# Performance work log

Measured on AMD Instinct MI355X. Metric: run time of the kernel, lower is better.

The kernel has to match this reference:

```python
import jax, jax.numpy as jnp
import numpy as np

B, T, D, U = 32, 512, 512, 512  # batch, seq_len, input dim, lstm units


def setup_inputs() -> dict:
    key = jax.random.key(0)
    ks = jax.random.split(key, 8)
    s_in = 1.0 / np.sqrt(D)
    s_rec = 1.0 / np.sqrt(U)
    return {
        "x": jax.random.normal(ks[0], (B, T, D), dtype=jnp.float32),
        "z": jax.random.normal(ks[1], (B, U), dtype=jnp.float32) * 0.1,
        # forward-direction LSTM params (Keras gate order: i, f, c, o)
        "Wf": jax.random.normal(ks[2], (D, 4 * U), dtype=jnp.float32) * s_in,
        "Uf": jax.random.normal(ks[3], (U, 4 * U), dtype=jnp.float32) * s_rec,
        "bf": jnp.zeros((4 * U,), dtype=jnp.float32),
        # backward-direction LSTM params
        "Wb": jax.random.normal(ks[4], (D, 4 * U), dtype=jnp.float32) * s_in,
        "Ub": jax.random.normal(ks[5], (U, 4 * U), dtype=jnp.float32) * s_rec,
        "bb": jnp.zeros((4 * U,), dtype=jnp.float32),
    }


def _lstm(x, h0, c0, W, Uw, b, reverse):
    """Single-direction LSTM, return_sequences=True. Keras gate order i,f,c,o."""
    u = h0.shape[-1]
    # precompute input projections for all timesteps in one big GEMM
    xg = jnp.einsum("btd,dk->btk", x, W) + b  # [B,T,4U]

    def step(carry, xg_t):
        h, c = carry
        g = xg_t + h @ Uw  # [B,4U]
        i = jax.nn.sigmoid(g[:, :u])
        f = jax.nn.sigmoid(g[:, u:2 * u])
        cc = jnp.tanh(g[:, 2 * u:3 * u])
        o = jax.nn.sigmoid(g[:, 3 * u:])
        c = f * c + i * cc
        h = o * jnp.tanh(c)
        return (h, c), h

    # scan over time; reverse=True == Keras go_backwards + output re-reversal
    _, hs = jax.lax.scan(step, (h0, c0), jnp.swapaxes(xg, 0, 1), reverse=reverse)
    return jnp.swapaxes(hs, 0, 1)  # [B,T,U]


def reference(x, z, Wf, Uf, bf, Wb, Ub, bb):
    # conditional=True: initial_state = [z, z, z, z] -> both directions get (h0=z, c0=z)
    fwd = _lstm(x, z, z, Wf, Uf, bf, reverse=False)
    bwd = _lstm(x, z, z, Wb, Ub, bb, reverse=True)
    return fwd + bwd  # Bidirectional merge_mode='sum', return_sequences=True
```

## Files before the change

### kernel.cpp

```cpp
#include <hip/hip_runtime.h>
#include <hip/hip_bf16.h>


typedef __attribute__((ext_vector_type(8))) __bf16 bf16x8;
typedef __attribute__((ext_vector_type(4))) __bf16 bf16x4;
typedef __attribute__((ext_vector_type(4))) float fvec4;

#define AS_G(p) ((const __attribute__((address_space(1))) void*)(p))
#define AS_L(p) ((__attribute__((address_space(3))) void*)(p))

__device__ __forceinline__ float sigm(float x) {
  return __builtin_amdgcn_rcpf(1.f + __expf(-x));
}
__device__ __forceinline__ float tanh_f(float x) {
  return 1.f - 2.f * __builtin_amdgcn_rcpf(__expf(2.f * x) + 1.f);
}

__device__ __forceinline__ void st_h4(__bf16* p, float h0, float h1) {
  union { __bf16 h[2]; unsigned int u; } pk;
  pk.h[0] = (__bf16)h0;
  pk.h[1] = (__bf16)h1;
  __hip_atomic_store((unsigned int*)p, pk.u, __ATOMIC_RELAXED, __HIP_MEMORY_SCOPE_AGENT);
}


__global__ void k_convert_x(const float* __restrict__ x, __bf16* __restrict__ xb) {
  size_t i = ((size_t)blockIdx.x * 256 + threadIdx.x) * 8;
  fvec4 a = *(const fvec4*)(x + i);
  fvec4 b = *(const fvec4*)(x + i + 4);
  bf16x8 o;
#pragma unroll
  for (int j = 0; j < 4; ++j) { o[j] = (__bf16)a[j]; o[4 + j] = (__bf16)b[j]; }
  *(bf16x8*)(xb + i) = o;
}

__global__ void k_build_T(const float* __restrict__ src, const float* __restrict__ bvec,
                          __bf16* __restrict__ dst, float* __restrict__ bias_out) {
  int p = blockIdx.x;
  int g = p >> 6, r = p & 63, w = r >> 4, q = r & 15, jj = q >> 2, gate = q & 3;
  int orig = gate * 512 + g * 16 + w * 4 + jj;
  for (int k = threadIdx.x; k < 512; k += 256)
    dst[(size_t)p * 512 + k] = (__bf16)src[(size_t)k * 2048 + orig];
  if (bias_out && threadIdx.x == 0) bias_out[p] = bvec[orig];
}

__global__ void k_init_flags(int* mbox) {
  int i = blockIdx.x * 256 + threadIdx.x;
  if (i < 2048) mbox[i] = 0;
}

__global__ void k_init_h(const float* __restrict__ z, __bf16* __restrict__ hbuf) {
  int idx = blockIdx.x * 256 + threadIdx.x;
  int dir = idx >> 14, rem = idx & 16383;
  int ks = rem >> 10, row = (rem >> 5) & 31, c = rem & 31;
  hbuf[(size_t)dir * 32768 + rem] = (__bf16)z[row * 512 + ks * 32 + c];
}


__global__ __launch_bounds__(256, 2) void k_gemm_xw(
    const __bf16* __restrict__ A,
    const __bf16* __restrict__ Bt,
    const float* __restrict__ bias,
    __bf16* __restrict__ C)
{
  __shared__ __align__(16) __bf16 As[128 * 32];
  __shared__ __align__(16) __bf16 Bs[128 * 32];
  const int tid = threadIdx.x;
  const int w = tid >> 6, lane = tid & 63, quad = lane >> 4, l15 = lane & 15;
  const int m0 = blockIdx.y * 128, n0 = blockIdx.x * 128;
  const int wm = w & 1, wn = w >> 1;

  fvec4 acc[4][4];
  const fvec4 zero = {0.f, 0.f, 0.f, 0.f};
#pragma unroll
  for (int i = 0; i < 4; ++i)
#pragma unroll
    for (int j = 0; j < 4; ++j) acc[i][j] = zero;

  for (int kb = 0; kb < 16; ++kb) {
    const int k0 = kb * 32;
#pragma unroll
    for (int i = 0; i < 2; ++i) {
      const int c = (i * 4 + w) * 64 + lane;
      const int row = c >> 2, kk = (c & 3) * 8;
      __builtin_amdgcn_global_load_lds(AS_G(A + (size_t)(m0 + row) * 512 + k0 + kk),
                                       AS_L(As + (size_t)(i * 4 + w) * 512), 16, 0, 0);
      __builtin_amdgcn_global_load_lds(AS_G(Bt + (size_t)(n0 + row) * 512 + k0 + kk),
                                       AS_L(Bs + (size_t)(i * 4 + w) * 512), 16, 0, 0);
    }
    __syncthreads();
    bf16x8 af[4], bfr[4];
#pragma unroll
    for (int mt = 0; mt < 4; ++mt)
      af[mt] = *(const bf16x8*)(As + (wm * 64 + mt * 16 + l15) * 32 + quad * 8);
#pragma unroll
    for (int nt = 0; nt < 4; ++nt)
      bfr[nt] = *(const bf16x8*)(Bs + (wn * 64 + nt * 16 + l15) * 32 + quad * 8);
#pragma unroll
    for (int mt = 0; mt < 4; ++mt)
#pragma unroll
      for (int nt = 0; nt < 4; ++nt)
        acc[mt][nt] = __builtin_amdgcn_mfma_f32_16x16x32_bf16(af[mt], bfr[nt], acc[mt][nt], 0, 0, 0);
    __syncthreads();
  }

#pragma unroll
  for (int nt = 0; nt < 4; ++nt) {
    const int col = n0 + wn * 64 + nt * 16 + l15;
    const float bv = bias[col];
#pragma unroll
    for (int mt = 0; mt < 4; ++mt) {
      const int rowb = m0 + wm * 64 + mt * 16 + quad * 4;
#pragma unroll
      for (int r = 0; r < 4; ++r)
        C[(size_t)(rowb + r) * 4096 + col] = (__bf16)(acc[mt][nt][r] + bv);
    }
  }
}


__global__ __launch_bounds__(256, 1) void k_lstm_rec(
    const __bf16* __restrict__ xg,
    const float* __restrict__ z,
    const __bf16* __restrict__ UT,
    __bf16* __restrict__ hbuf,
    float* __restrict__ outf,
    __bf16* __restrict__ outb,
    int* __restrict__ mbox)
{
  const int blk = blockIdx.x, dir = blk >> 5, g = blk & 31;
  const int tid = threadIdx.x, w = tid >> 6, lane = tid & 63;
  const int quad = lane >> 4, l15 = lane & 15;
  __shared__ __align__(16) __bf16 h_lds[16384];
  __shared__ __align__(16) float gates[32][68];

  bf16x8 breg[16];
  {
    const __bf16* up = UT + ((size_t)dir * 2048 + g * 64 + w * 16 + l15) * 512 + quad * 8;
#pragma unroll
    for (int ks = 0; ks < 16; ++ks) breg[ks] = *(const bf16x8*)(up + ks * 32);
  }

  const int b = lane >> 1, jpair = lane & 1;
  const int hcol = g * 16 + w * 4 + jpair * 2;
  float c0 = z[b * 512 + hcol];
  float c1 = z[b * 512 + hcol + 1];
  const __bf16* hsrc = hbuf + (size_t)dir * 32768;
  const int stoff = (g >> 1) * 1024 + b * 32 + (g & 1) * 16 + w * 4 + jpair * 2;
  const int stage_off = w * 4096 + lane * 8;
  const int swz8 = ((lane & 3) ^ ((lane >> 3) & 3)) * 8;
  const int fr_swz = ((l15 >> 1) & 3);
  int* my_line = mbox + dir * 1024 + g * 32;
  int* my_col  = mbox + dir * 1024 + lane * 32 + g;
  const fvec4 zero = {0.f, 0.f, 0.f, 0.f};

  for (int kt = 0; kt < 512; ++kt) {
    const int t = dir ? (511 - kt) : kt;
    const int pr = kt & 1;

    const bf16x8 xv = *(const bf16x8*)(xg + (size_t)(b * 512 + t) * 4096 +
                                       dir * 2048 + g * 64 + w * 16 + jpair * 8);

    if (kt > 0) {
      if (w == 0) {
        const int* mb = my_line + (lane & 31);
        for (;;) {
          int v = __hip_atomic_load(mb, __ATOMIC_RELAXED, __HIP_MEMORY_SCOPE_AGENT);
          if (!__ballot(lane < 32 && v < kt)) break;
          __builtin_amdgcn_s_sleep(1);
        }
      }
      __syncthreads();
    }

    {
      const unsigned long long* src =
          (const unsigned long long*)(hsrc + pr * 16384 + stage_off);
      unsigned long long tmp[16];
#pragma unroll
      for (int it = 0; it < 8; ++it) {
        tmp[2 * it]     = __hip_atomic_load(src + it * 128,
                            __ATOMIC_RELAXED, __HIP_MEMORY_SCOPE_AGENT);
        tmp[2 * it + 1] = __hip_atomic_load(src + it * 128 + 1,
                            __ATOMIC_RELAXED, __HIP_MEMORY_SCOPE_AGENT);
      }
#pragma unroll
      for (int it = 0; it < 8; ++it) {
        union { unsigned long long u[2]; bf16x8 v; } cv;
        cv.u[0] = tmp[2 * it];
        cv.u[1] = tmp[2 * it + 1];
        *(bf16x8*)(h_lds + (w * 4 + (it >> 1)) * 1024 +
                   ((it & 1) * 16 + (lane >> 2)) * 32 + swz8) = cv.v;
      }
    }
    __syncthreads();

    fvec4 acc0 = zero, acc1 = zero;
#pragma unroll 8
    for (int ks = 0; ks < 16; ++ks) {
      bf16x8 a0 = *(const bf16x8*)(h_lds + ks * 1024 + l15 * 32 +
                                   ((quad ^ fr_swz) * 8));
      bf16x8 a1 = *(const bf16x8*)(h_lds + ks * 1024 + (16 + l15) * 32 +
                                   ((quad ^ fr_swz) * 8));
      acc0 = __builtin_amdgcn_mfma_f32_16x16x32_bf16(a0, breg[ks], acc0, 0, 0, 0);
      acc1 = __builtin_amdgcn_mfma_f32_16x16x32_bf16(a1, breg[ks], acc1, 0, 0, 0);
    }

#pragma unroll
    for (int r = 0; r < 4; ++r) {
      gates[quad * 4 + r][w * 16 + l15] = acc0[r];
      gates[16 + quad * 4 + r][w * 16 + l15] = acc1[r];
    }
    const fvec4 gA = *(const fvec4*)&gates[b][w * 16 + jpair * 8];
    const fvec4 gB = *(const fvec4*)&gates[b][w * 16 + jpair * 8 + 4];

    float xf[8];
#pragma unroll
    for (int j = 0; j < 8; ++j) xf[j] = (float)xv[j];

    float ii = sigm(gA[0] + xf[0]);
    float ff = sigm(gA[1] + xf[1]);
    float cc = tanh_f(gA[2] + xf[2]);
    float oo = sigm(gA[3] + xf[3]);
    c0 = ff * c0 + ii * cc;
    const float h0 = oo * tanh_f(c0);

    ii = sigm(gB[0] + xf[4]);
    ff = sigm(gB[1] + xf[5]);
    cc = tanh_f(gB[2] + xf[6]);
    oo = sigm(gB[3] + xf[7]);
    c1 = ff * c1 + ii * cc;
    const float h1 = oo * tanh_f(c1);

    st_h4(hbuf + (size_t)dir * 32768 + ((kt + 1) & 1) * 16384 + stoff, h0, h1);

    __syncthreads();
    if (w == 0 && lane < 32)
      __hip_atomic_store(my_col, kt + 1, __ATOMIC_RELAXED, __HIP_MEMORY_SCOPE_AGENT);

    const size_t oidx = (size_t)(b * 512 + t) * 512 + hcol;
    if (dir == 0) {
      outf[oidx] = h0;
      outf[oidx + 1] = h1;
    } else {
      outb[oidx] = (__bf16)h0;
      outb[oidx + 1] = (__bf16)h1;
    }
  }
}


__global__ void k_add_bwd(float* __restrict__ out, const __bf16* __restrict__ outb) {
  size_t i = ((size_t)blockIdx.x * 256 + threadIdx.x) * 4;
  if (i >= (size_t)32 * 512 * 512) return;
  fvec4 o = *(const fvec4*)(out + i);
  bf16x4 bv = *(const bf16x4*)(outb + i);
#pragma unroll
  for (int j = 0; j < 4; ++j) o[j] += (float)bv[j];
  *(fvec4*)(out + i) = o;
}


extern "C" void kernel_launch(void* const* d_in, const int* in_sizes, int n_in,
                              void* d_out, int out_size, void* d_ws, size_t ws_size,
                              hipStream_t stream) {
  const float* x  = (const float*)d_in[0];
  const float* z  = (const float*)d_in[1];
  const float* Wf = (const float*)d_in[2];
  const float* Uf = (const float*)d_in[3];
  const float* bf = (const float*)d_in[4];
  const float* Wb = (const float*)d_in[5];
  const float* Ub = (const float*)d_in[6];
  const float* bb = (const float*)d_in[7];
  float* out = (float*)d_out;
  char* ws = (char*)d_ws;

  size_t off = 0;
  __bf16* xg    = (__bf16*)(ws + off); off += (size_t)16384 * 4096 * 2;
  __bf16* UT    = (__bf16*)(ws + off); off += (size_t)2 * 2048 * 512 * 2;
  __bf16* hbuf  = (__bf16*)(ws + off); off += (size_t)2 * 2 * 16384 * 2;
  int*    mbox  = (int*)(ws + off);    off += 8192;
  float*  biasp = (float*)(ws + off);  off += 4096 * 4;
  char* uni = ws + off;
  __bf16* xb   = (__bf16*)uni;
  __bf16* WT   = (__bf16*)(uni + (size_t)16384 * 512 * 2);
  __bf16* outb = (__bf16*)uni;

  k_convert_x<<<4096, 256, 0, stream>>>(x, xb);
  k_build_T<<<2048, 256, 0, stream>>>(Wf, bf, WT, biasp);
  k_build_T<<<2048, 256, 0, stream>>>(Wb, bb, WT + (size_t)2048 * 512, biasp + 2048);
  k_build_T<<<2048, 256, 0, stream>>>(Uf, nullptr, UT, nullptr);
  k_build_T<<<2048, 256, 0, stream>>>(Ub, nullptr, UT + (size_t)2048 * 512, nullptr);
  k_init_flags<<<8, 256, 0, stream>>>(mbox);
  k_init_h<<<128, 256, 0, stream>>>(z, hbuf);
  k_gemm_xw<<<dim3(32, 128), 256, 0, stream>>>(xb, WT, biasp, xg);
  k_lstm_rec<<<64, 256, 0, stream>>>(xg, z, UT, hbuf, out, outb, mbox);
  k_add_bwd<<<8192, 256, 0, stream>>>(out, outb);
}
```

Baseline: 2.205 ms.

## Replace flag mailbox sync with step-tagged h values in recurrent LSTM kernel

Drops the separate per-block flag mailbox and the extra barrier-then-flag-store handshake. Each 64-bit store now carries the packed bf16 h pair together with the timestep counter, so consumers poll the data words directly until every tag matches the expected step. This takes a polling round trip and a __syncthreads off each of the 512 serial steps. In exchange the exchanged buffer doubles in size, every thread spins on 32 global loads per step, and the LDS layout changes to a padded, unswizzled one that may bring bank conflicts.

Result: slower. 2.770 ms (+25.6%).

```diff
diff --git a/kernel.cpp b/kernel.cpp
--- a/kernel.cpp
+++ b/kernel.cpp
@@ -5,6 +5,7 @@
 typedef __attribute__((ext_vector_type(8))) __bf16 bf16x8;
 typedef __attribute__((ext_vector_type(4))) __bf16 bf16x4;
 typedef __attribute__((ext_vector_type(4))) float fvec4;
+typedef __attribute__((ext_vector_type(2))) float fvec2;
 
 #define AS_G(p) ((const __attribute__((address_space(1))) void*)(p))
 #define AS_L(p) ((__attribute__((address_space(3))) void*)(p))
@@ -14,13 +15,6 @@
 }
 __device__ __forceinline__ float tanh_f(float x) {
   return 1.f - 2.f * __builtin_amdgcn_rcpf(__expf(2.f * x) + 1.f);
-}
-
-__device__ __forceinline__ void st_h4(__bf16* p, float h0, float h1) {
-  union { __bf16 h[2]; unsigned int u; } pk;
-  pk.h[0] = (__bf16)h0;
-  pk.h[1] = (__bf16)h1;
-  __hip_atomic_store((unsigned int*)p, pk.u, __ATOMIC_RELAXED, __HIP_MEMORY_SCOPE_AGENT);
 }
 
 
@@ -44,16 +38,19 @@
   if (bias_out && threadIdx.x == 0) bias_out[p] = bvec[orig];
 }
 
-__global__ void k_init_flags(int* mbox) {
-  int i = blockIdx.x * 256 + threadIdx.x;
-  if (i < 2048) mbox[i] = 0;
-}
-
-__global__ void k_init_h(const float* __restrict__ z, __bf16* __restrict__ hbuf) {
+__global__ void k_init_rec(const float* __restrict__ z,
+                           unsigned long long* __restrict__ rbuf) {
   int idx = blockIdx.x * 256 + threadIdx.x;
-  int dir = idx >> 14, rem = idx & 16383;
-  int ks = rem >> 10, row = (rem >> 5) & 31, c = rem & 31;
-  hbuf[(size_t)dir * 32768 + rem] = (__bf16)z[row * 512 + ks * 32 + c];
+  int par = (idx >> 13) & 1;
+  int ks = (idx >> 9) & 15, row = (idx >> 4) & 31, cp = idx & 15;
+  unsigned long long v = 0ull;
+  if (par == 0) {
+    union { __bf16 h[2]; unsigned u; } pk;
+    pk.h[0] = (__bf16)z[row * 512 + ks * 32 + cp * 2];
+    pk.h[1] = (__bf16)z[row * 512 + ks * 32 + cp * 2 + 1];
+    v = (unsigned long long)pk.u;
+  }
+  rbuf[idx] = v;
 }
 
 
@@ -123,15 +120,14 @@
     const __bf16* __restrict__ xg,
     const float* __restrict__ z,
     const __bf16* __restrict__ UT,
-    __bf16* __restrict__ hbuf,
+    unsigned long long* __restrict__ rbuf,
     float* __restrict__ outf,
-    __bf16* __restrict__ outb,
-    int* __restrict__ mbox)
+    __bf16* __restrict__ outb)
 {
   const int blk = blockIdx.x, dir = blk >> 5, g = blk & 31;
   const int tid = threadIdx.x, w = tid >> 6, lane = tid & 63;
   const int quad = lane >> 4, l15 = lane & 15;
-  __shared__ __align__(16) __bf16 h_lds[16384];
+  __shared__ __align__(16) char h_lds[16 * 2080];
   __shared__ __align__(16) float gates[32][68];
 
   bf16x8 breg[16];
@@ -145,63 +141,50 @@
   const int hcol = g * 16 + w * 4 + jpair * 2;
   float c0 = z[b * 512 + hcol];
   float c1 = z[b * 512 + hcol + 1];
-  const __bf16* hsrc = hbuf + (size_t)dir * 32768;
-  const int stoff = (g >> 1) * 1024 + b * 32 + (g & 1) * 16 + w * 4 + jpair * 2;
-  const int stage_off = w * 4096 + lane * 8;
-  const int swz8 = ((lane & 3) ^ ((lane >> 3) & 3)) * 8;
-  const int fr_swz = ((l15 >> 1) & 3);
-  int* my_line = mbox + dir * 1024 + g * 32;
-  int* my_col  = mbox + dir * 1024 + lane * 32 + g;
-  const fvec4 zero = {0.f, 0.f, 0.f, 0.f};
+
+  const int ks_s = tid >> 4, cp = tid & 15;
+  unsigned long long* rb_dir = rbuf + (size_t)dir * 16384;
+  unsigned long long* src_base = rb_dir + ks_s * 512 + cp;
+  const int pidx = (g >> 1) * 512 + b * 16 + (g & 1) * 8 + w * 2 + jpair;
 
   for (int kt = 0; kt < 512; ++kt) {
     const int t = dir ? (511 - kt) : kt;
     const int pr = kt & 1;
 
+    asm volatile("s_waitcnt lgkmcnt(0)\n\ts_barrier" ::: "memory");
+
     const bf16x8 xv = *(const bf16x8*)(xg + (size_t)(b * 512 + t) * 4096 +
                                        dir * 2048 + g * 64 + w * 16 + jpair * 8);
 
-    if (kt > 0) {
-      if (w == 0) {
-        const int* mb = my_line + (lane & 31);
-        for (;;) {
-          int v = __hip_atomic_load(mb, __ATOMIC_RELAXED, __HIP_MEMORY_SCOPE_AGENT);
-          if (!__ballot(lane < 32 && v < kt)) break;
-          __builtin_amdgcn_s_sleep(1);
-        }
+    unsigned long long rec[32];
+    {
+      unsigned long long* srcp = src_base + pr * 8192;
+      const unsigned expect = (unsigned)kt;
+      for (;;) {
+#pragma unroll
+        for (int it = 0; it < 32; ++it)
+          rec[it] = __hip_atomic_load(srcp + it * 16, __ATOMIC_RELAXED,
+                                      __HIP_MEMORY_SCOPE_AGENT);
+        asm volatile("s_waitcnt vmcnt(0)" ::: "memory");
+        unsigned ok = 1u;
+#pragma unroll
+        for (int it = 0; it < 32; ++it)
+          ok &= (unsigned)((unsigned)(rec[it] >> 32) == expect);
+        if (__all((int)ok)) break;
+        __builtin_amdgcn_s_sleep(1);
       }
-      __syncthreads();
-    }
-
-    {
-      const unsigned long long* src =
-          (const unsigned long long*)(hsrc + pr * 16384 + stage_off);
-      unsigned long long tmp[16];
-#pragma unroll
-      for (int it = 0; it < 8; ++it) {
-        tmp[2 * it]     = __hip_atomic_load(src + it * 128,
-                            __ATOMIC_RELAXED, __HIP_MEMORY_SCOPE_AGENT);
-        tmp[2 * it + 1] = __hip_atomic_load(src + it * 128 + 1,
-                            __ATOMIC_RELAXED, __HIP_MEMORY_SCOPE_AGENT);
-      }
-#pragma unroll
-      for (int it = 0; it < 8; ++it) {
-        union { unsigned long long u[2]; bf16x8 v; } cv;
-        cv.u[0] = tmp[2 * it];
-        cv.u[1] = tmp[2 * it + 1];
-        *(bf16x8*)(h_lds + (w * 4 + (it >> 1)) * 1024 +
-                   ((it & 1) * 16 + (lane >> 2)) * 32 + swz8) = cv.v;
-      }
-    }
-    __syncthreads();
-
-    fvec4 acc0 = zero, acc1 = zero;
+    }
+#pragma unroll
+    for (int it = 0; it < 32; ++it)
+      *(unsigned*)(h_lds + ks_s * 2080 + it * 64 + cp * 4) = (unsigned)rec[it];
+
+    asm volatile("s_waitcnt lgkmcnt(0)\n\ts_barrier" ::: "memory");
+
+    fvec4 acc0 = {0.f, 0.f, 0.f, 0.f}, acc1 = {0.f, 0.f, 0.f, 0.f};
 #pragma unroll 8
     for (int ks = 0; ks < 16; ++ks) {
-      bf16x8 a0 = *(const bf16x8*)(h_lds + ks * 1024 + l15 * 32 +
-                                   ((quad ^ fr_swz) * 8));
-      bf16x8 a1 = *(const bf16x8*)(h_lds + ks * 1024 + (16 + l15) * 32 +
-                                   ((quad ^ fr_swz) * 8));
+      bf16x8 a0 = *(const bf16x8*)(h_lds + ks * 2080 + l15 * 64 + quad * 16);
+      bf16x8 a1 = *(const bf16x8*)(h_lds + ks * 2080 + 1024 + l15 * 64 + quad * 16);
       acc0 = __builtin_amdgcn_mfma_f32_16x16x32_bf16(a0, breg[ks], acc0, 0, 0, 0);
       acc1 = __builtin_amdgcn_mfma_f32_16x16x32_bf16(a1, breg[ks], acc1, 0, 0, 0);
     }
@@ -232,19 +215,20 @@
     c1 = ff * c1 + ii * cc;
     const float h1 = oo * tanh_f(c1);
 
-    st_h4(hbuf + (size_t)dir * 32768 + ((kt + 1) & 1) * 16384 + stoff, h0, h1);
-
-    __syncthreads();
-    if (w == 0 && lane < 32)
-      __hip_atomic_store(my_col, kt + 1, __ATOMIC_RELAXED, __HIP_MEMORY_SCOPE_AGENT);
+    union { __bf16 h[2]; unsigned u; } pk;
+    pk.h[0] = (__bf16)h0;
+    pk.h[1] = (__bf16)h1;
+    const unsigned long long rv =
+        (unsigned long long)pk.u | ((unsigned long long)(unsigned)(kt + 1) << 32);
+    __hip_atomic_store(rb_dir + ((kt + 1) & 1) * 8192 + pidx, rv,
+                       __ATOMIC_RELAXED, __HIP_MEMORY_SCOPE_AGENT);
 
     const size_t oidx = (size_t)(b * 512 + t) * 512 + hcol;
     if (dir == 0) {
-      outf[oidx] = h0;
-      outf[oidx + 1] = h1;
+      fvec2 ov = {h0, h1};
+      *(fvec2*)(outf + oidx) = ov;
     } else {
-      outb[oidx] = (__bf16)h0;
-      outb[oidx + 1] = (__bf16)h1;
+      *(unsigned*)(outb + oidx) = pk.u;
     }
   }
 }
@@ -276,11 +260,11 @@
   char* ws = (char*)d_ws;
 
   size_t off = 0;
-  __bf16* xg    = (__bf16*)(ws + off); off += (size_t)16384 * 4096 * 2;
-  __bf16* UT    = (__bf16*)(ws + off); off += (size_t)2 * 2048 * 512 * 2;
-  __bf16* hbuf  = (__bf16*)(ws + off); off += (size_t)2 * 2 * 16384 * 2;
-  int*    mbox  = (int*)(ws + off);    off += 8192;
-  float*  biasp = (float*)(ws + off);  off += 4096 * 4;
+  __bf16* xg = (__bf16*)(ws + off); off += (size_t)16384 * 4096 * 2;
+  __bf16* UT = (__bf16*)(ws + off); off += (size_t)2 * 2048 * 512 * 2;
+  unsigned long long* rbuf = (unsigned long long*)(ws + off);
+  off += (size_t)2 * 2 * 8192 * 8;
+  float* biasp = (float*)(ws + off); off += 4096 * 4;
   char* uni = ws + off;
   __bf16* xb   = (__bf16*)uni;
   __bf16* WT   = (__bf16*)(uni + (size_t)16384 * 512 * 2);
@@ -291,9 +275,8 @@
   k_build_T<<<2048, 256, 0, stream>>>(Wb, bb, WT + (size_t)2048 * 512, biasp + 2048);
   k_build_T<<<2048, 256, 0, stream>>>(Uf, nullptr, UT, nullptr);
   k_build_T<<<2048, 256, 0, stream>>>(Ub, nullptr, UT + (size_t)2048 * 512, nullptr);
-  k_init_flags<<<8, 256, 0, stream>>>(mbox);
-  k_init_h<<<128, 256, 0, stream>>>(z, hbuf);
+  k_init_rec<<<128, 256, 0, stream>>>(z, rbuf);
   k_gemm_xw<<<dim3(32, 128), 256, 0, stream>>>(xb, WT, biasp, xg);
-  k_lstm_rec<<<64, 256, 0, stream>>>(xg, z, UT, hbuf, out, outb, mbox);
+  k_lstm_rec<<<64, 256, 0, stream>>>(xg, z, UT, rbuf, out, outb);
   k_add_bwd<<<8192, 256, 0, stream>>>(out, outb);
 }
```
